# Kernel tuning notes

Hardware: AMD Instinct MI355X
Metric: run time of the kernel (lower is better)

The kernel has to match this reference:

```python
import jax, jax.numpy as jnp
import numpy as np

B, H, L, N = 16, 256, 4096, 64
N2 = N // 2  # conjugate-pair parameterization: keep half the state modes


def setup_inputs() -> dict:
    key = jax.random.key(0)
    ks = jax.random.split(key, 12)
    x = jax.random.normal(ks[0], (B, H, L), jnp.float32)
    # BatchNorm1d params + running stats (inference mode)
    g1 = jnp.ones((H,), jnp.float32); b1 = jnp.zeros((H,), jnp.float32)
    m1 = 0.1 * jax.random.normal(ks[1], (H,), jnp.float32)
    v1 = 1.0 + 0.1 * jax.random.uniform(ks[2], (H,), jnp.float32)
    g2 = jnp.ones((H,), jnp.float32); b2 = jnp.zeros((H,), jnp.float32)
    m2 = 0.1 * jax.random.normal(ks[3], (H,), jnp.float32)
    v2 = 1.0 + 0.1 * jax.random.uniform(ks[4], (H,), jnp.float32)
    # S4 SSM kernel parameters (S4D-Lin init); bidirectional -> 2 channels of C
    log_dt = jnp.log(1e-3) + (jnp.log(1e-1) - jnp.log(1e-3)) * jax.random.uniform(ks[5], (H,), jnp.float32)
    logA_re = jnp.log(0.5) * jnp.ones((H, N2), jnp.float32)  # A_real = -exp(logA_re) = -0.5
    A_im = jnp.pi * jnp.broadcast_to(jnp.arange(N2, dtype=jnp.float32), (H, N2))
    C_re = jax.random.normal(ks[6], (2, H, N2), jnp.float32) * np.float32(0.5 ** 0.5)
    C_im = jax.random.normal(ks[7], (2, H, N2), jnp.float32) * np.float32(0.5 ** 0.5)
    D = jax.random.normal(ks[8], (H,), jnp.float32)  # skip term
    # S4 output linear: Conv1d(H, 2H, 1) followed by GLU
    Wo = jax.random.normal(ks[9], (2 * H, H), jnp.float32) / np.float32(np.sqrt(H))
    bo = jnp.zeros((2 * H,), jnp.float32)
    # FFN 1x1 convs
    W2 = jax.random.normal(ks[10], (2 * H, H), jnp.float32) / np.float32(np.sqrt(H))
    b2f = jnp.zeros((2 * H,), jnp.float32)
    W3 = jax.random.normal(ks[11], (H, 2 * H), jnp.float32) / np.float32(np.sqrt(2 * H))
    b3 = jnp.zeros((H,), jnp.float32)
    return dict(x=x, g1=g1, b1=b1, m1=m1, v1=v1, log_dt=log_dt, logA_re=logA_re,
                A_im=A_im, C_re=C_re, C_im=C_im, D=D, Wo=Wo, bo=bo,
                g2=g2, b2=b2, m2=m2, v2=v2, W2=W2, b2f=b2f, W3=W3, b3=b3)


def _bn(x, g, b, m, v, eps=1e-5):
    # inference-mode BatchNorm1d over channel dim of (B, H, L)
    scale = g / jnp.sqrt(v + eps)
    return (x - m[:, None]) * scale[:, None] + b[:, None]


def _s4(x, log_dt, logA_re, A_im, C_re, C_im, D, Wo, bo):
    # x: (B, H, L). Bidirectional diagonal SSM via FFT convolution.
    Ln = x.shape[-1]
    Hh = x.shape[1]
    dt = jnp.exp(log_dt)                               # (H,)
    A = -jnp.exp(logA_re) + 1j * A_im                  # (H, N2)
    dtA = dt[:, None] * A                              # (H, N2)
    C = (C_re + 1j * C_im) * (jnp.exp(dtA) - 1.0) / A  # (2, H, N2) ZOH discretization
    vand = jnp.exp(dtA[:, :, None] * jnp.arange(Ln))   # (H, N2, L) Vandermonde
    k = 2.0 * jnp.einsum('chn,hnl->chl', C, vand).real  # (2, H, L) fwd/bwd kernels
    k_fwd, k_bwd = k[0], k[1]
    zpad = jnp.zeros_like(k_fwd)
    k_full = (jnp.concatenate([k_fwd, zpad], axis=-1)
              + jnp.concatenate([zpad, k_bwd[:, ::-1]], axis=-1))  # (H, 2L)
    u_f = jnp.fft.rfft(x, n=2 * Ln)
    k_f = jnp.fft.rfft(k_full, n=2 * Ln)
    y = jnp.fft.irfft(u_f * k_f, n=2 * Ln)[..., :Ln]   # (B, H, L)
    y = y + D[:, None] * x                             # skip connection
    y = jax.nn.gelu(y, approximate=False)
    z = jnp.einsum('oi,bil->bol', Wo, y) + bo[:, None]  # (B, 2H, L)
    return z[:, :Hh] * jax.nn.sigmoid(z[:, Hh:])        # GLU -> (B, H, L)


def reference(x, g1, b1, m1, v1, log_dt, logA_re, A_im, C_re, C_im, D, Wo, bo,
              g2, b2, m2, v2, W2, b2f, W3, b3):
    # residual 1: BN -> S4 -> add
    res = x
    h = _bn(x, g1, b1, m1, v1)
    h = _s4(h, log_dt, logA_re, A_im, C_re, C_im, D, Wo, bo)
    x = res + h
    # residual 2: BN -> conv1x1(H->2H) -> GELU -> conv1x1(2H->H) -> add
    res = x
    h = _bn(x, g2, b2, m2, v2)
    h = jnp.einsum('oi,bil->bol', W2, h) + b2f[:, None]
    h = jax.nn.gelu(h, approximate=False)
    h = jnp.einsum('oi,bil->bol', W3, h) + b3[:, None]
    return res + h
```

## Files before the change

### kernel.cpp

```cpp
#include <hip/hip_runtime.h>

#define BB 16
#define HH 256
#define LL 4096
#define NN2 32

static constexpr float BN_EPS = 1e-5f;

__device__ __forceinline__ float gelu_exact(float v) {
    return 0.5f * v * (1.0f + erff(v * 0.70710678118654752f));
}
__device__ __forceinline__ float sigmoidf_(float v) {
    return 1.0f / (1.0f + expf(-v));
}

__global__ void k_consts(const float* __restrict__ log_dt,
                         const float* __restrict__ logA_re,
                         const float* __restrict__ A_im,
                         const float* __restrict__ C_re,
                         const float* __restrict__ C_im,
                         float* __restrict__ cst) {
    int idx = blockIdx.x * blockDim.x + threadIdx.x;
    if (idx >= HH * NN2) return;
    int h = idx / NN2;
    float dt = expf(log_dt[h]);
    float Ar = -expf(logA_re[idx]);
    float Ai = A_im[idx];
    float er = expf(dt * Ar);
    float wr = er * cosf(dt * Ai);
    float wi = er * sinf(dt * Ai);
    float Er = wr - 1.0f, Ei = wi;
    float inv = 1.0f / (Ar * Ar + Ai * Ai);
    float Fr = (Er * Ar + Ei * Ai) * inv;
    float Fi = (Ei * Ar - Er * Ai) * inv;
    cst[idx] = wr;
    cst[8192 + idx] = wi;
    #pragma unroll
    for (int c = 0; c < 2; ++c) {
        float Cr = C_re[c * HH * NN2 + idx], Ci = C_im[c * HH * NN2 + idx];
        cst[8192 * (2 + 2 * c) + idx] = 2.0f * (Cr * Fr - Ci * Fi);
        cst[8192 * (3 + 2 * c) + idx] = 2.0f * (Cr * Fi + Ci * Fr);
    }
}

__global__ __launch_bounds__(64) void k_scan(const float* __restrict__ x,
                                             const float* __restrict__ g1,
                                             const float* __restrict__ b1,
                                             const float* __restrict__ m1,
                                             const float* __restrict__ v1,
                                             const float* __restrict__ cst,
                                             float* __restrict__ yf,
                                             float* __restrict__ yb) {
    __shared__ float smem[2368];
    int bh = blockIdx.x;
    int h = bh & (HH - 1);
    int lane = threadIdx.x;
    int half = lane >> 5;
    int n = lane & 31;
    int hn = h * NN2 + n;

    float wr = cst[hn];
    float wi = cst[8192 + hn];
    float Cr = cst[8192 * (2 + 2 * half) + hn];
    float Ci = cst[8192 * (3 + 2 * half) + hn];

    float sc = g1[h] * rsqrtf(v1[h] + BN_EPS);
    float sh = fmaf(-m1[h], sc, b1[h]);

    const float* xrow = x + (size_t)bh * LL;
    float* yfr = yf + (size_t)bh * LL;
    float* ybr = yb + (size_t)bh * LL;

    float sr = 0.0f, si = 0.0f;
    const int hbase = half * 1152;
    const int xsw = (n >> 3) << 2;
    const int lbase = hbase + n * 36;
    const int xbase = 2304 + half * 32;

    float xraw = half ? xrow[LL - 1 - n] : xrow[n];

    for (int c = 0; c < LL / 32; ++c) {
        smem[xbase + n] = fmaf(xraw, sc, sh);
        if (c + 1 < LL / 32) {
            int gnext = (c + 1) * 32 + n;
            xraw = half ? xrow[LL - 1 - gnext] : xrow[gnext];
        }
        __syncthreads();

        #pragma unroll
        for (int j = 0; j < 32; j += 4) {
            float4 xq = *(const float4*)&smem[xbase + j];
            float4 cb;
            { float t0 = fmaf(wr, sr, xq.x); float ns = fmaf(wi, sr, wr * si);
              sr = fmaf(-wi, si, t0); si = ns; cb.x = fmaf(Cr, sr, -(Ci * si)); }
            { float t0 = fmaf(wr, sr, xq.y); float ns = fmaf(wi, sr, wr * si);
              sr = fmaf(-wi, si, t0); si = ns; cb.y = fmaf(Cr, sr, -(Ci * si)); }
            { float t0 = fmaf(wr, sr, xq.z); float ns = fmaf(wi, sr, wr * si);
              sr = fmaf(-wi, si, t0); si = ns; cb.z = fmaf(Cr, sr, -(Ci * si)); }
            { float t0 = fmaf(wr, sr, xq.w); float ns = fmaf(wi, sr, wr * si);
              sr = fmaf(-wi, si, t0); si = ns; cb.w = fmaf(Cr, sr, -(Ci * si)); }
            *(float4*)&smem[lbase + (j ^ xsw)] = cb;
        }
        __syncthreads();

        float s0 = 0.0f, s1 = 0.0f, s2 = 0.0f, s3 = 0.0f;
        #pragma unroll
        for (int m = 0; m < 32; m += 4) {
            s0 += smem[hbase + (m + 0) * 36 + (n ^ (((m + 0) >> 3) << 2))];
            s1 += smem[hbase + (m + 1) * 36 + (n ^ (((m + 1) >> 3) << 2))];
            s2 += smem[hbase + (m + 2) * 36 + (n ^ (((m + 2) >> 3) << 2))];
            s3 += smem[hbase + (m + 3) * 36 + (n ^ (((m + 3) >> 3) << 2))];
        }
        float sum = (s0 + s1) + (s2 + s3);
        int gl = c * 32 + n;
        if (half) {
            int oidx = LL - 2 - gl;
            if (oidx >= 0) ybr[oidx] = sum;
        } else {
            yfr[gl] = sum;
        }
    }
}

__global__ void k_combine(const float* __restrict__ x,
                          const float* __restrict__ g1,
                          const float* __restrict__ b1,
                          const float* __restrict__ m1,
                          const float* __restrict__ v1,
                          const float* __restrict__ D,
                          const float* __restrict__ yb,
                          float* __restrict__ y) {
    int i4 = blockIdx.x * blockDim.x + threadIdx.x;
    if (i4 >= BB * HH * LL / 4) return;
    int row = i4 >> 10;
    int h = row & (HH - 1);
    float sc = g1[h] * rsqrtf(v1[h] + BN_EPS);
    float sh = fmaf(-m1[h], sc, b1[h]);
    float d = D[h];
    float4 xv = ((const float4*)x)[i4];
    float4 yv = ((float4*)y)[i4];
    float4 bv = ((const float4*)yb)[i4];
    if ((i4 & 1023) == 1023) bv.w = 0.0f;
    yv.x = gelu_exact(fmaf(d, fmaf(xv.x, sc, sh), yv.x + bv.x));
    yv.y = gelu_exact(fmaf(d, fmaf(xv.y, sc, sh), yv.y + bv.y));
    yv.z = gelu_exact(fmaf(d, fmaf(xv.z, sc, sh), yv.z + bv.z));
    yv.w = gelu_exact(fmaf(d, fmaf(xv.w, sc, sh), yv.w + bv.w));
    ((float4*)y)[i4] = yv;
}

template <int MODE>
__global__ __launch_bounds__(256) void k_gemm(const float* __restrict__ A,
                                              const float* __restrict__ Bm,
                                              const float* __restrict__ bias,
                                              const float* __restrict__ X,
                                              const float* __restrict__ bng,
                                              const float* __restrict__ bnb,
                                              const float* __restrict__ bnm,
                                              const float* __restrict__ bnv,
                                              float* __restrict__ Out) {
    constexpr int K  = (MODE == 2) ? 512 : 256;
    constexpr int CH = (MODE == 2) ? 512 : 256;
    constexpr int OC = (MODE == 1) ? 512 : 256;

    __shared__ float As[32][128];
    __shared__ float Bs[32][64];

    int tid = threadIdx.x;
    int tx = tid & 15, ty = tid >> 4;
    int gm = blockIdx.x;
    int l0 = blockIdx.y * 64;
    int b  = blockIdx.z;

    int lm = tid & 127;
    int kg = (tid >> 7) << 4;
    int grow;
    if (MODE == 0) grow = (lm < 64) ? (gm * 64 + lm) : (256 + gm * 64 + (lm - 64));
    else           grow = gm * 128 + lm;
    const float* arow = A + (size_t)grow * K + kg;

    int bl = (tid & 15) * 4;
    int bk = tid >> 4;

    float acc[2][4][4] = {};

    for (int k0 = 0; k0 < K; k0 += 32) {
        float4 av[4];
        #pragma unroll
        for (int t = 0; t < 4; ++t) av[t] = *(const float4*)(arow + k0 + t * 4);

        const float* brow0 = Bm + ((size_t)b * CH + k0 + bk) * LL + l0 + bl;
        float4 bv0 = *(const float4*)brow0;
        float4 bv1 = *(const float4*)(brow0 + (size_t)16 * LL);
        if (MODE == 1) {
            int i0 = k0 + bk, i1 = i0 + 16;
            float s0 = bng[i0] * rsqrtf(bnv[i0] + BN_EPS);
            float h0 = fmaf(-bnm[i0], s0, bnb[i0]);
            float s1 = bng[i1] * rsqrtf(bnv[i1] + BN_EPS);
            float h1 = fmaf(-bnm[i1], s1, bnb[i1]);
            bv0.x = fmaf(bv0.x, s0, h0); bv0.y = fmaf(bv0.y, s0, h0);
            bv0.z = fmaf(bv0.z, s0, h0); bv0.w = fmaf(bv0.w, s0, h0);
            bv1.x = fmaf(bv1.x, s1, h1); bv1.y = fmaf(bv1.y, s1, h1);
            bv1.z = fmaf(bv1.z, s1, h1); bv1.w = fmaf(bv1.w, s1, h1);
        }

        __syncthreads();
        #pragma unroll
        for (int t = 0; t < 4; ++t) {
            As[kg + t * 4 + 0][lm] = av[t].x;
            As[kg + t * 4 + 1][lm] = av[t].y;
            As[kg + t * 4 + 2][lm] = av[t].z;
            As[kg + t * 4 + 3][lm] = av[t].w;
        }
        *(float4*)&Bs[bk][bl]      = bv0;
        *(float4*)&Bs[bk + 16][bl] = bv1;
        __syncthreads();

        #pragma unroll
        for (int kk = 0; kk < 32; ++kk) {
            float4 a0 = *(const float4*)&As[kk][ty * 4];
            float4 a1 = *(const float4*)&As[kk][64 + ty * 4];
            float4 bq = *(const float4*)&Bs[kk][tx * 4];
            float a0v[4] = {a0.x, a0.y, a0.z, a0.w};
            float a1v[4] = {a1.x, a1.y, a1.z, a1.w};
            float bqv[4] = {bq.x, bq.y, bq.z, bq.w};
            #pragma unroll
            for (int rr = 0; rr < 4; ++rr)
                #pragma unroll
                for (int cc = 0; cc < 4; ++cc) {
                    acc[0][rr][cc] = fmaf(a0v[rr], bqv[cc], acc[0][rr][cc]);
                    acc[1][rr][cc] = fmaf(a1v[rr], bqv[cc], acc[1][rr][cc]);
                }
        }
    }

    #pragma unroll
    for (int rr = 0; rr < 4; ++rr) {
        if (MODE == 0) {
            int o1 = gm * 64 + ty * 4 + rr;
            size_t oi = ((size_t)b * OC + o1) * LL + l0 + tx * 4;
            float bz1 = bias[o1], bz2 = bias[o1 + 256];
            float4 xr = *(const float4*)(X + oi);
            float4 r;
            r.x = xr.x + (acc[0][rr][0] + bz1) * sigmoidf_(acc[1][rr][0] + bz2);
            r.y = xr.y + (acc[0][rr][1] + bz1) * sigmoidf_(acc[1][rr][1] + bz2);
            r.z = xr.z + (acc[0][rr][2] + bz1) * sigmoidf_(acc[1][rr][2] + bz2);
            r.w = xr.w + (acc[0][rr][3] + bz1) * sigmoidf_(acc[1][rr][3] + bz2);
            *(float4*)(Out + oi) = r;
        } else if (MODE == 1) {
            int o0 = gm * 128 + ty * 4 + rr;
            #pragma unroll
            for (int hf = 0; hf < 2; ++hf) {
                int o = o0 + hf * 64;
                size_t oi = ((size_t)b * OC + o) * LL + l0 + tx * 4;
                float bz = bias[o];
                float4 r;
                r.x = gelu_exact(acc[hf][rr][0] + bz);
                r.y = gelu_exact(acc[hf][rr][1] + bz);
                r.z = gelu_exact(acc[hf][rr][2] + bz);
                r.w = gelu_exact(acc[hf][rr][3] + bz);
                *(float4*)(Out + oi) = r;
            }
        } else {
            int o0 = gm * 128 + ty * 4 + rr;
            #pragma unroll
            for (int hf = 0; hf < 2; ++hf) {
                int o = o0 + hf * 64;
                size_t oi = ((size_t)b * OC + o) * LL + l0 + tx * 4;
                float bz = bias[o];
                float4 xr = *(const float4*)(X + oi);
                float4 r;
                r.x = xr.x + acc[hf][rr][0] + bz;
                r.y = xr.y + acc[hf][rr][1] + bz;
                r.z = xr.z + acc[hf][rr][2] + bz;
                r.w = xr.w + acc[hf][rr][3] + bz;
                *(float4*)(Out + oi) = r;
            }
        }
    }
}

extern "C" void kernel_launch(void* const* d_in, const int* in_sizes, int n_in,
                              void* d_out, int out_size, void* d_ws, size_t ws_size,
                              hipStream_t stream) {
    const float* x       = (const float*)d_in[0];
    const float* g1      = (const float*)d_in[1];
    const float* b1      = (const float*)d_in[2];
    const float* m1      = (const float*)d_in[3];
    const float* v1      = (const float*)d_in[4];
    const float* log_dt  = (const float*)d_in[5];
    const float* logA_re = (const float*)d_in[6];
    const float* A_im    = (const float*)d_in[7];
    const float* C_re    = (const float*)d_in[8];
    const float* C_im    = (const float*)d_in[9];
    const float* D       = (const float*)d_in[10];
    const float* Wo      = (const float*)d_in[11];
    const float* bo      = (const float*)d_in[12];
    const float* g2      = (const float*)d_in[13];
    const float* b2      = (const float*)d_in[14];
    const float* m2      = (const float*)d_in[15];
    const float* v2      = (const float*)d_in[16];
    const float* W2      = (const float*)d_in[17];
    const float* b2f     = (const float*)d_in[18];
    const float* W3      = (const float*)d_in[19];
    const float* b3      = (const float*)d_in[20];
    float* out = (float*)d_out;

    char* wsb = (char*)d_ws;
    float* yf   = (float*)wsb;
    float* yb   = (float*)(wsb + (size_t)64 * 1024 * 1024);
    float* h2   = (float*)wsb;
    float* cst  = (float*)(wsb + (size_t)128 * 1024 * 1024);

    k_consts<<<dim3(HH * NN2 / 256), dim3(256), 0, stream>>>(log_dt, logA_re, A_im, C_re, C_im, cst);
    k_scan<<<dim3(BB * HH), dim3(64), 0, stream>>>(x, g1, b1, m1, v1, cst, yf, yb);
    k_combine<<<dim3(BB * HH * LL / 4 / 256), dim3(256), 0, stream>>>(x, g1, b1, m1, v1, D, yb, yf);
    k_gemm<0><<<dim3(4, 64, 16), dim3(256), 0, stream>>>(Wo, yf, bo, x,
                                                         nullptr, nullptr, nullptr, nullptr, out);
    k_gemm<1><<<dim3(4, 64, 16), dim3(256), 0, stream>>>(W2, out, b2f, nullptr,
                                                         g2, b2, m2, v2, h2);
    k_gemm<2><<<dim3(2, 64, 16), dim3(256), 0, stream>>>(W3, h2, b3, out,
                                                         nullptr, nullptr, nullptr, nullptr, out);
}
```

Before: 1.073 ms.

## Run 1x1-conv GEMMs on bf16 MFMA with split hi/lo precision emulation

```diff
diff --git a/kernel.cpp b/kernel.cpp
--- a/kernel.cpp
+++ b/kernel.cpp
@@ -5,6 +5,9 @@
 #define LL 4096
 #define NN2 32
 
+using f32x16 = __attribute__((ext_vector_type(16))) float;
+using bfx8   = __attribute__((ext_vector_type(8))) short;
+
 static constexpr float BN_EPS = 1e-5f;
 
 __device__ __forceinline__ float gelu_exact(float v) {
@@ -12,6 +15,17 @@
 }
 __device__ __forceinline__ float sigmoidf_(float v) {
     return 1.0f / (1.0f + expf(-v));
+}
+__device__ __forceinline__ ushort f2bf(float f) {
+    uint u = __float_as_uint(f);
+    u += 0x7fffu + ((u >> 16) & 1u);
+    return (ushort)(u >> 16);
+}
+__device__ __forceinline__ float bf2f(ushort h) {
+    return __uint_as_float(((uint)h) << 16);
+}
+__device__ __forceinline__ int rowstart(int l) {
+    return l * 12 + ((l >> 3) & 7) * 4 + ((l >> 6) << 5);
 }
 
 __global__ void k_consts(const float* __restrict__ log_dt,
@@ -43,6 +57,37 @@
     }
 }
 
+__global__ void k_prep2a(const float* __restrict__ g2, const float* __restrict__ b2,
+                         const float* __restrict__ m2, const float* __restrict__ v2,
+                         float* __restrict__ s2, float* __restrict__ t2) {
+    int k = threadIdx.x;
+    float s = g2[k] * rsqrtf(v2[k] + BN_EPS);
+    s2[k] = s;
+    t2[k] = fmaf(-m2[k], s, b2[k]);
+}
+__global__ void k_prep2b(const float* __restrict__ W2, const float* __restrict__ t2,
+                         const float* __restrict__ b2f, float* __restrict__ bias2p) {
+    int o = blockIdx.x * 256 + threadIdx.x;
+    float acc = b2f[o];
+    for (int k = 0; k < 256; ++k) acc = fmaf(W2[o * 256 + k], t2[k], acc);
+    bias2p[o] = acc;
+}
+__global__ void k_wprep(const float* __restrict__ Wo, const float* __restrict__ W2,
+                        const float* __restrict__ W3, const float* __restrict__ s2,
+                        ushort* __restrict__ WoH, ushort* __restrict__ WoL,
+                        ushort* __restrict__ W2H, ushort* __restrict__ W2L,
+                        ushort* __restrict__ W3H, ushort* __restrict__ W3L) {
+    int i = blockIdx.x * 256 + threadIdx.x;
+    int job = i >> 17, e = i & 131071;
+    float w; ushort *H, *L;
+    if (job == 0)      { w = Wo[e];                  H = WoH; L = WoL; }
+    else if (job == 1) { w = W2[e] * s2[e & 255];    H = W2H; L = W2L; }
+    else               { w = W3[e];                  H = W3H; L = W3L; }
+    ushort h = f2bf(w);
+    H[e] = h;
+    L[e] = f2bf(w - bf2f(h));
+}
+
 __global__ __launch_bounds__(64) void k_scan(const float* __restrict__ x,
                                              const float* __restrict__ g1,
                                              const float* __restrict__ b1,
@@ -123,13 +168,10 @@
 }
 
 __global__ void k_combine(const float* __restrict__ x,
-                          const float* __restrict__ g1,
-                          const float* __restrict__ b1,
-                          const float* __restrict__ m1,
-                          const float* __restrict__ v1,
+                          const float* __restrict__ g1, const float* __restrict__ b1,
+                          const float* __restrict__ m1, const float* __restrict__ v1,
                           const float* __restrict__ D,
-                          const float* __restrict__ yb,
-                          float* __restrict__ y) {
+                          const float* __restrict__ yb, float* __restrict__ y) {
     int i4 = blockIdx.x * blockDim.x + threadIdx.x;
     if (i4 >= BB * HH * LL / 4) return;
     int row = i4 >> 10;
@@ -148,6 +190,185 @@
     ((float4*)y)[i4] = yv;
 }
 
+__global__ void k_combine2(const float* __restrict__ x,
+                           const float* __restrict__ g1, const float* __restrict__ b1,
+                           const float* __restrict__ m1, const float* __restrict__ v1,
+                           const float* __restrict__ D,
+                           const float* __restrict__ yf, const float* __restrict__ yb,
+                           ushort* __restrict__ s4h, ushort* __restrict__ s4l) {
+    int i4 = blockIdx.x * blockDim.x + threadIdx.x;
+    if (i4 >= BB * HH * LL / 4) return;
+    int row = i4 >> 10;
+    int h = row & (HH - 1);
+    float sc = g1[h] * rsqrtf(v1[h] + BN_EPS);
+    float sh = fmaf(-m1[h], sc, b1[h]);
+    float d = D[h];
+    float4 xv = ((const float4*)x)[i4];
+    float4 fv = ((const float4*)yf)[i4];
+    float4 bv = ((const float4*)yb)[i4];
+    if ((i4 & 1023) == 1023) bv.w = 0.0f;
+    float v0 = gelu_exact(fmaf(d, fmaf(xv.x, sc, sh), fv.x + bv.x));
+    float v1_ = gelu_exact(fmaf(d, fmaf(xv.y, sc, sh), fv.y + bv.y));
+    float v2 = gelu_exact(fmaf(d, fmaf(xv.z, sc, sh), fv.z + bv.z));
+    float v3 = gelu_exact(fmaf(d, fmaf(xv.w, sc, sh), fv.w + bv.w));
+    ushort4 hh, ll;
+    hh.x = f2bf(v0);  ll.x = f2bf(v0 - bf2f(hh.x));
+    hh.y = f2bf(v1_); ll.y = f2bf(v1_ - bf2f(hh.y));
+    hh.z = f2bf(v2);  ll.z = f2bf(v2 - bf2f(hh.z));
+    hh.w = f2bf(v3);  ll.w = f2bf(v3 - bf2f(hh.w));
+    ((ushort4*)s4h)[i4] = hh;
+    ((ushort4*)s4l)[i4] = ll;
+}
+
+template <int MODE>
+__global__ __launch_bounds__(256) void k_mgemm(
+    const ushort* __restrict__ Ah, const ushort* __restrict__ Al,
+    const ushort* __restrict__ Bh, const ushort* __restrict__ Bl,
+    const float* __restrict__ bias,
+    const float* __restrict__ X,
+    float* __restrict__ Outf,
+    ushort* __restrict__ Oh, ushort* __restrict__ Ol) {
+
+    constexpr int K  = (MODE == 2) ? 512 : 256;
+    constexpr int NK = K / 16;
+
+    __shared__ uint bt[3200];
+    __shared__ float gatebuf[(MODE == 0) ? 8192 : 4];
+
+    const int tid  = threadIdx.x;
+    const int lane = tid & 63;
+    const int w    = tid >> 6;
+    const int c31  = lane & 31;
+    const int g    = lane >> 5;
+    const int gm   = blockIdx.x;
+    const int l0   = blockIdx.y * 128;
+    const int b    = blockIdx.z;
+
+    int r = w * 32 + c31;
+    int arow;
+    if (MODE == 0) arow = (r < 64) ? (gm * 64 + r) : (256 + gm * 64 + (r - 64));
+    else           arow = gm * 128 + r;
+    const ushort* apH = Ah + (size_t)arow * K;
+    const ushort* apL = Al + (size_t)arow * K;
+
+    const int pl = tid >> 7;
+    const int tt = tid & 127;
+    const int kp = tt & 7;
+    const int lg = tt >> 3;
+    const ushort* bplane = pl ? Bl : Bh;
+    const ushort* bbase = bplane + ((size_t)b * K + 2 * kp) * LL + l0 + lg * 8;
+    uint* btp = bt + pl * 1600;
+    const int wb = 96 * lg + 4 * (lg & 7) + 32 * (lg >> 3);
+    const int sl0 = (kp & 3) + 4 * (kp >> 2);
+    const int sl1 = (kp & 3) + 4 * ((kp >> 2) ^ 1);
+
+    f32x16 acc[4];
+    #pragma unroll
+    for (int f = 0; f < 4; ++f)
+        #pragma unroll
+        for (int e = 0; e < 16; ++e) acc[f][e] = 0.0f;
+
+    uint4 r0 = *(const uint4*)(bbase);
+    uint4 r1 = *(const uint4*)(bbase + LL);
+
+    for (int kc = 0; kc < NK; ++kc) {
+        __syncthreads();
+        {
+            uint p0 = (r0.x & 0xffffu) | (r1.x << 16);
+            uint p1 = (r0.x >> 16)     | (r1.x & 0xffff0000u);
+            uint p2 = (r0.y & 0xffffu) | (r1.y << 16);
+            uint p3 = (r0.y >> 16)     | (r1.y & 0xffff0000u);
+            uint p4 = (r0.z & 0xffffu) | (r1.z << 16);
+            uint p5 = (r0.z >> 16)     | (r1.z & 0xffff0000u);
+            uint p6 = (r0.w & 0xffffu) | (r1.w << 16);
+            uint p7 = (r0.w >> 16)     | (r1.w & 0xffff0000u);
+            btp[wb +  0 + sl0] = p0;
+            btp[wb + 12 + sl1] = p1;
+            btp[wb + 24 + sl0] = p2;
+            btp[wb + 36 + sl1] = p3;
+            btp[wb + 48 + sl0] = p4;
+            btp[wb + 60 + sl1] = p5;
+            btp[wb + 72 + sl0] = p6;
+            btp[wb + 84 + sl1] = p7;
+        }
+        __syncthreads();
+        if (kc + 1 < NK) {
+            const ushort* nb = bbase + (size_t)((kc + 1) * 16) * LL;
+            r0 = *(const uint4*)(nb);
+            r1 = *(const uint4*)(nb + LL);
+        }
+        bfx8 ah = *(const bfx8*)(apH + kc * 16 + 8 * g);
+        bfx8 al = *(const bfx8*)(apL + kc * 16 + 8 * g);
+        #pragma unroll
+        for (int f = 0; f < 4; ++f) {
+            int l = f * 32 + c31;
+            int ra = rowstart(l) + ((g ^ (l & 1)) << 2);
+            bfx8 bhf = *(const bfx8*)(bt + ra);
+            bfx8 blf = *(const bfx8*)(bt + 1600 + ra);
+            acc[f] = __builtin_amdgcn_mfma_f32_32x32x16_bf16(ah, bhf, acc[f], 0, 0, 0);
+            acc[f] = __builtin_amdgcn_mfma_f32_32x32x16_bf16(ah, blf, acc[f], 0, 0, 0);
+            acc[f] = __builtin_amdgcn_mfma_f32_32x32x16_bf16(al, bhf, acc[f], 0, 0, 0);
+        }
+    }
+
+    if (MODE == 0) {
+        if (w >= 2) {
+            int grow_base = (w - 2) * 32;
+            int og_base = 256 + gm * 64 + grow_base;
+            #pragma unroll
+            for (int f = 0; f < 4; ++f)
+                #pragma unroll
+                for (int reg = 0; reg < 16; ++reg) {
+                    int rr = (reg & 3) + 8 * (reg >> 2) + 4 * g;
+                    float zg = acc[f][reg] + bias[og_base + rr];
+                    gatebuf[(grow_base + rr) * 128 + f * 32 + c31] = sigmoidf_(zg);
+                }
+        }
+        __syncthreads();
+        if (w < 2) {
+            int vr_base = w * 32;
+            #pragma unroll
+            for (int f = 0; f < 4; ++f)
+                #pragma unroll
+                for (int reg = 0; reg < 16; ++reg) {
+                    int rr = (reg & 3) + 8 * (reg >> 2) + 4 * g;
+                    int vr = vr_base + rr;
+                    int ov = gm * 64 + vr;
+                    size_t oi = ((size_t)b * HH + ov) * LL + l0 + f * 32 + c31;
+                    float zv = acc[f][reg] + bias[ov];
+                    float res = X[oi] + zv * gatebuf[vr * 128 + f * 32 + c31];
+                    Outf[oi] = res;
+                    ushort hh = f2bf(res);
+                    Oh[oi] = hh;
+                    Ol[oi] = f2bf(res - bf2f(hh));
+                }
+        }
+    } else if (MODE == 1) {
+        #pragma unroll
+        for (int f = 0; f < 4; ++f)
+            #pragma unroll
+            for (int reg = 0; reg < 16; ++reg) {
+                int rr = (reg & 3) + 8 * (reg >> 2) + 4 * g;
+                int o = gm * 128 + w * 32 + rr;
+                size_t oi = ((size_t)b * 512 + o) * LL + l0 + f * 32 + c31;
+                float v = gelu_exact(acc[f][reg] + bias[o]);
+                ushort hh = f2bf(v);
+                Oh[oi] = hh;
+                Ol[oi] = f2bf(v - bf2f(hh));
+            }
+    } else {
+        #pragma unroll
+        for (int f = 0; f < 4; ++f)
+            #pragma unroll
+            for (int reg = 0; reg < 16; ++reg) {
+                int rr = (reg & 3) + 8 * (reg >> 2) + 4 * g;
+                int o = gm * 128 + w * 32 + rr;
+                size_t oi = ((size_t)b * HH + o) * LL + l0 + f * 32 + c31;
+                Outf[oi] = Outf[oi] + acc[f][reg] + bias[o];
+            }
+    }
+}
+
 template <int MODE>
 __global__ __launch_bounds__(256) void k_gemm(const float* __restrict__ A,
                                               const float* __restrict__ Bm,
@@ -240,12 +461,12 @@
             size_t oi = ((size_t)b * OC + o1) * LL + l0 + tx * 4;
             float bz1 = bias[o1], bz2 = bias[o1 + 256];
             float4 xr = *(const float4*)(X + oi);
-            float4 r;
-            r.x = xr.x + (acc[0][rr][0] + bz1) * sigmoidf_(acc[1][rr][0] + bz2);
-            r.y = xr.y + (acc[0][rr][1] + bz1) * sigmoidf_(acc[1][rr][1] + bz2);
-            r.z = xr.z + (acc[0][rr][2] + bz1) * sigmoidf_(acc[1][rr][2] + bz2);
-            r.w = xr.w + (acc[0][rr][3] + bz1) * sigmoidf_(acc[1][rr][3] + bz2);
-            *(float4*)(Out + oi) = r;
+            float4 rv;
+            rv.x = xr.x + (acc[0][rr][0] + bz1) * sigmoidf_(acc[1][rr][0] + bz2);
+            rv.y = xr.y + (acc[0][rr][1] + bz1) * sigmoidf_(acc[1][rr][1] + bz2);
+            rv.z = xr.z + (acc[0][rr][2] + bz1) * sigmoidf_(acc[1][rr][2] + bz2);
+            rv.w = xr.w + (acc[0][rr][3] + bz1) * sigmoidf_(acc[1][rr][3] + bz2);
+            *(float4*)(Out + oi) = rv;
         } else if (MODE == 1) {
             int o0 = gm * 128 + ty * 4 + rr;
             #pragma unroll
@@ -253,12 +474,12 @@
                 int o = o0 + hf * 64;
                 size_t oi = ((size_t)b * OC + o) * LL + l0 + tx * 4;
                 float bz = bias[o];
-                float4 r;
-                r.x = gelu_exact(acc[hf][rr][0] + bz);
-                r.y = gelu_exact(acc[hf][rr][1] + bz);
-                r.z = gelu_exact(acc[hf][rr][2] + bz);
-                r.w = gelu_exact(acc[hf][rr][3] + bz);
-                *(float4*)(Out + oi) = r;
+                float4 rv;
+                rv.x = gelu_exact(acc[hf][rr][0] + bz);
+                rv.y = gelu_exact(acc[hf][rr][1] + bz);
+                rv.z = gelu_exact(acc[hf][rr][2] + bz);
+                rv.w = gelu_exact(acc[hf][rr][3] + bz);
+                *(float4*)(Out + oi) = rv;
             }
         } else {
             int o0 = gm * 128 + ty * 4 + rr;
@@ -268,12 +489,12 @@
                 size_t oi = ((size_t)b * OC + o) * LL + l0 + tx * 4;
                 float bz = bias[o];
                 float4 xr = *(const float4*)(X + oi);
-                float4 r;
-                r.x = xr.x + acc[hf][rr][0] + bz;
-                r.y = xr.y + acc[hf][rr][1] + bz;
-                r.z = xr.z + acc[hf][rr][2] + bz;
-                r.w = xr.w + acc[hf][rr][3] + bz;
-                *(float4*)(Out + oi) = r;
+                float4 rv;
+                rv.x = xr.x + acc[hf][rr][0] + bz;
+                rv.y = xr.y + acc[hf][rr][1] + bz;
+                rv.z = xr.z + acc[hf][rr][2] + bz;
+                rv.w = xr.w + acc[hf][rr][3] + bz;
+                *(float4*)(Out + oi) = rv;
             }
         }
     }
@@ -304,20 +525,54 @@
     const float* W3      = (const float*)d_in[19];
     const float* b3      = (const float*)d_in[20];
     float* out = (float*)d_out;
-
     char* wsb = (char*)d_ws;
-    float* yf   = (float*)wsb;
-    float* yb   = (float*)(wsb + (size_t)64 * 1024 * 1024);
-    float* h2   = (float*)wsb;
-    float* cst  = (float*)(wsb + (size_t)128 * 1024 * 1024);
-
-    k_consts<<<dim3(HH * NN2 / 256), dim3(256), 0, stream>>>(log_dt, logA_re, A_im, C_re, C_im, cst);
-    k_scan<<<dim3(BB * HH), dim3(64), 0, stream>>>(x, g1, b1, m1, v1, cst, yf, yb);
-    k_combine<<<dim3(BB * HH * LL / 4 / 256), dim3(256), 0, stream>>>(x, g1, b1, m1, v1, D, yb, yf);
-    k_gemm<0><<<dim3(4, 64, 16), dim3(256), 0, stream>>>(Wo, yf, bo, x,
-                                                         nullptr, nullptr, nullptr, nullptr, out);
-    k_gemm<1><<<dim3(4, 64, 16), dim3(256), 0, stream>>>(W2, out, b2f, nullptr,
-                                                         g2, b2, m2, v2, h2);
-    k_gemm<2><<<dim3(2, 64, 16), dim3(256), 0, stream>>>(W3, h2, b3, out,
-                                                         nullptr, nullptr, nullptr, nullptr, out);
-}
+
+    const size_t MB = 1024 * 1024;
+    const size_t NEEDED = 194 * MB;
+
+    if (ws_size >= NEEDED) {
+        float*  cst    = (float*)wsb;
+        float*  s2     = (float*)(wsb + 196608);
+        float*  t2     = (float*)(wsb + 197632);
+        float*  bias2p = (float*)(wsb + 198656);
+        ushort* WoH = (ushort*)(wsb + 262144);
+        ushort* WoL = (ushort*)(wsb + 524288);
+        ushort* W2H = (ushort*)(wsb + 786432);
+        ushort* W2L = (ushort*)(wsb + 1048576);
+        ushort* W3H = (ushort*)(wsb + 1310720);
+        ushort* W3L = (ushort*)(wsb + 1572864);
+        float*  yf  = (float*)(wsb + 2 * MB);
+        float*  yb  = (float*)(wsb + 66 * MB);
+        ushort* s4h = (ushort*)(wsb + 130 * MB);
+        ushort* s4l = (ushort*)(wsb + 162 * MB);
+        ushort* x1h = (ushort*)(wsb + 2 * MB);
+        ushort* x1l = (ushort*)(wsb + 34 * MB);
+        ushort* h2h = (ushort*)(wsb + 66 * MB);
+        ushort* h2l = (ushort*)(wsb + 130 * MB);
+
+        k_consts<<<dim3(HH * NN2 / 256), dim3(256), 0, stream>>>(log_dt, logA_re, A_im, C_re, C_im, cst);
+        k_prep2a<<<dim3(1), dim3(256), 0, stream>>>(g2, b2, m2, v2, s2, t2);
+        k_wprep<<<dim3(1536), dim3(256), 0, stream>>>(Wo, W2, W3, s2, WoH, WoL, W2H, W2L, W3H, W3L);
+        k_prep2b<<<dim3(2), dim3(256), 0, stream>>>(W2, t2, b2f, bias2p);
+        k_scan<<<dim3(BB * HH), dim3(64), 0, stream>>>(x, g1, b1, m1, v1, cst, yf, yb);
+        k_combine2<<<dim3(BB * HH * LL / 4 / 256), dim3(256), 0, stream>>>(x, g1, b1, m1, v1, D, yf, yb, s4h, s4l);
+        k_mgemm<0><<<dim3(4, 32, 16), dim3(256), 0, stream>>>(WoH, WoL, s4h, s4l, bo, x, out, x1h, x1l);
+        k_mgemm<1><<<dim3(4, 32, 16), dim3(256), 0, stream>>>(W2H, W2L, x1h, x1l, bias2p, nullptr, nullptr, h2h, h2l);
+        k_mgemm<2><<<dim3(2, 32, 16), dim3(256), 0, stream>>>(W3H, W3L, h2h, h2l, b3, nullptr, out, nullptr, nullptr);
+    } else {
+        float* yf  = (float*)wsb;
+        float* yb  = (float*)(wsb + 64 * MB);
+        float* h2  = (float*)wsb;
+        float* cst = (float*)(wsb + 128 * MB);
+
+        k_consts<<<dim3(HH * NN2 / 256), dim3(256), 0, stream>>>(log_dt, logA_re, A_im, C_re, C_im, cst);
+        k_scan<<<dim3(BB * HH), dim3(64), 0, stream>>>(x, g1, b1, m1, v1, cst, yf, yb);
+        k_combine<<<dim3(BB * HH * LL / 4 / 256), dim3(256), 0, stream>>>(x, g1, b1, m1, v1, D, yb, yf);
+        k_gemm<0><<<dim3(4, 64, 16), dim3(256), 0, stream>>>(Wo, yf, bo, x,
+                                                             nullptr, nullptr, nullptr, nullptr, out);
+        k_gemm<1><<<dim3(4, 64, 16), dim3(256), 0, stream>>>(W2, out, b2f, nullptr,
+                                                             g2, b2, m2, v2, h2);
+        k_gemm<2><<<dim3(2, 64, 16), dim3(256), 0, stream>>>(W3, h2, b3, out,
+                                                             nullptr, nullptr, nullptr, nullptr, out);
+    }
+}
```

New measurement: 982.1 us. 8.5% less time.
